# Kernel tuning notes

Hardware: AMD Instinct MI355X
Metric: run time of the kernel (lower is better)

Reference implementation:

```python
import jax, jax.numpy as jnp
import numpy as np

S = 7
NUM_CLASSES = 20
BATCH = 16384


def _iou(a, b):
    # a, b: [..., 4] boxes in (cx, cy, w, h) format
    ax1, ay1 = a[..., 0] - a[..., 2] / 2, a[..., 1] - a[..., 3] / 2
    ax2, ay2 = a[..., 0] + a[..., 2] / 2, a[..., 1] + a[..., 3] / 2
    bx1, by1 = b[..., 0] - b[..., 2] / 2, b[..., 1] - b[..., 3] / 2
    bx2, by2 = b[..., 0] + b[..., 2] / 2, b[..., 1] + b[..., 3] / 2
    iw = jnp.clip(jnp.minimum(ax2, bx2) - jnp.maximum(ax1, bx1), 0.0)
    ih = jnp.clip(jnp.minimum(ay2, by2) - jnp.maximum(ay1, by1), 0.0)
    inter = iw * ih
    union = a[..., 2] * a[..., 3] + b[..., 2] * b[..., 3] - inter
    return inter / (union + 1e-10)


def setup_inputs() -> dict:
    key = jax.random.key(0)
    k1, k2, k3, k4 = jax.random.split(key, 4)
    preds = jax.random.uniform(k1, (BATCH, S, S, 30), jnp.float32, 0.05, 0.95)
    box = jax.random.uniform(k2, (BATCH, S, S, 4), jnp.float32, 0.05, 0.95)
    conf = jax.random.bernoulli(k3, 0.3, (BATCH, S, S, 1)).astype(jnp.float32)
    cls = jax.random.uniform(k4, (BATCH, S, S, NUM_CLASSES), jnp.float32)
    labels = jnp.concatenate([box, conf, box, conf, cls], axis=-1)
    return {"preds": preds, "labels": labels}


def reference(preds, labels):
    obj = labels[..., 4] == 1.0          # [N, S, S] responsible-cell mask
    obj_f = obj.astype(preds.dtype)
    noobj_f = 1.0 - obj_f

    iou1 = _iou(preds[..., 0:4], labels[..., 0:4])
    iou2 = _iou(preds[..., 5:9], labels[..., 0:4])
    b1 = iou1 > iou2                      # box 1 is responsible
    b1f = b1.astype(preds.dtype)[..., None]

    # responsible / other box slices selected per cell
    p_xy = b1f * preds[..., 0:2] + (1 - b1f) * preds[..., 5:7]
    l_xy = b1f * labels[..., 0:2] + (1 - b1f) * labels[..., 5:7]
    p_wh = b1f * preds[..., 2:4] + (1 - b1f) * preds[..., 7:9]
    l_wh = b1f * labels[..., 2:4] + (1 - b1f) * labels[..., 7:9]
    conf_resp = jnp.where(b1, preds[..., 4], preds[..., 9])
    conf_other = jnp.where(b1, preds[..., 9], preds[..., 4])
    iou_resp = jnp.where(b1, iou1, iou2)
    iou_other = jnp.where(b1, iou2, iou1)

    loss_xy = 5.0 * jnp.sum(obj_f * jnp.sum((p_xy - l_xy) ** 2, axis=-1))
    loss_wh = jnp.sum(obj_f * jnp.sum((jnp.sqrt(p_wh) - jnp.sqrt(l_wh)) ** 2, axis=-1))
    loss_obj = jnp.sum(obj_f * (conf_resp - iou_resp) ** 2)
    loss_noobj_in = 0.5 * jnp.sum(obj_f * (conf_other - iou_other) ** 2)
    loss_noobj_out = 0.5 * jnp.sum(noobj_f * (preds[..., 4] ** 2 + preds[..., 9] ** 2))
    loss_cls = jnp.sum(obj_f * jnp.sum((preds[..., 10:] - labels[..., 10:]) ** 2, axis=-1))

    total = loss_xy + loss_wh + loss_obj + loss_noobj_in + loss_noobj_out + loss_cls
    return total / preds.shape[0]
```

## Files before the change

kernel.cpp:

```cpp
#include <hip/hip_runtime.h>

#define S 7
#define NUM_CLASSES 20
#define BATCH 16384
#define NCELLS (BATCH * S * S)
#define CPB 128
#define NTILES (NCELLS / CPB)
#define BLOCK 64
#define GRID 512
#define TILE_FLOATS (CPB * 30)
#define GPL 15

__device__ __forceinline__ void async_load16(const float* g, float* s) {
    __builtin_amdgcn_global_load_lds(
        (const __attribute__((address_space(1))) void*)g,
        (__attribute__((address_space(3))) void*)s,
        16, 0, 0);
}

__device__ __forceinline__ float iou_f(float acx, float acy, float aw, float ah,
                                       float bcx, float bcy, float bw, float bh) {
    float ax1 = acx - aw * 0.5f, ay1 = acy - ah * 0.5f;
    float ax2 = acx + aw * 0.5f, ay2 = acy + ah * 0.5f;
    float bx1 = bcx - bw * 0.5f, by1 = bcy - bh * 0.5f;
    float bx2 = bcx + bw * 0.5f, by2 = bcy + bh * 0.5f;
    float iw = fminf(ax2, bx2) - fmaxf(ax1, bx1);
    iw = fmaxf(iw, 0.0f);
    float ih = fminf(ay2, by2) - fmaxf(ay1, by1);
    ih = fmaxf(ih, 0.0f);
    float inter = iw * ih;
    float uni = aw * ah + bw * bh - inter;
    return inter / (uni + 1e-10f);
}

__device__ __forceinline__ float cell_loss(const float* cp, const float* cl) {
    float p[30], l[30];
    const float2* pp = (const float2*)cp;
    const float2* ll = (const float2*)cl;
#pragma unroll
    for (int j = 0; j < 15; ++j) {
        float2 v = pp[j];
        p[2 * j] = v.x; p[2 * j + 1] = v.y;
        float2 w = ll[j];
        l[2 * j] = w.x; l[2 * j + 1] = w.y;
    }

    float obj = (l[4] == 1.0f) ? 1.0f : 0.0f;

    float iou1 = iou_f(p[0], p[1], p[2], p[3], l[0], l[1], l[2], l[3]);
    float iou2 = iou_f(p[5], p[6], p[7], p[8], l[0], l[1], l[2], l[3]);
    bool b1 = iou1 > iou2;

    float pxy0 = b1 ? p[0] : p[5];
    float pxy1 = b1 ? p[1] : p[6];
    float pwh0 = b1 ? p[2] : p[7];
    float pwh1 = b1 ? p[3] : p[8];
    float conf_resp  = b1 ? p[4] : p[9];
    float conf_other = b1 ? p[9] : p[4];
    float iou_resp   = b1 ? iou1 : iou2;
    float iou_other  = b1 ? iou2 : iou1;

    float dx = pxy0 - l[0];
    float dy = pxy1 - l[1];
    float loss_xy = dx * dx + dy * dy;

    float sw0 = sqrtf(pwh0) - sqrtf(l[2]);
    float sw1 = sqrtf(pwh1) - sqrtf(l[3]);
    float loss_wh = sw0 * sw0 + sw1 * sw1;

    float d_obj = conf_resp - iou_resp;
    float loss_obj = d_obj * d_obj;

    float d_no = conf_other - iou_other;
    float loss_noobj_in = 0.5f * d_no * d_no;

    float loss_noobj_out = 0.5f * (1.0f - obj) * (p[4] * p[4] + p[9] * p[9]);

    float loss_cls = 0.0f;
#pragma unroll
    for (int c = 10; c < 30; ++c) {
        float d = p[c] - l[c];
        loss_cls += d * d;
    }

    return obj * (5.0f * loss_xy + loss_wh + loss_obj + loss_noobj_in + loss_cls)
         + loss_noobj_out;
}

__global__ __launch_bounds__(BLOCK) void yolo_loss_kernel(
        const float* __restrict__ preds,
        const float* __restrict__ labels,
        float* __restrict__ out) {
    __shared__ __align__(16) float sp[2][TILE_FLOATS];
    __shared__ __align__(16) float sl[2][TILE_FLOATS];

    const int lane = threadIdx.x;
    float acc = 0.0f;

    const int f0 = lane * 4;

    int t = blockIdx.x;
    const int iters = (NTILES - (int)blockIdx.x + GRID - 1) / GRID;

    {
        const float* gp = preds  + (size_t)t * TILE_FLOATS;
        const float* gl = labels + (size_t)t * TILE_FLOATS;
#pragma unroll
        for (int it = 0; it < GPL; ++it) {
            int f = f0 + it * 256;
            async_load16(gp + f, &sp[0][f]);
            async_load16(gl + f, &sl[0][f]);
        }
    }

    int bb = 0;
    for (int i = 1; i < iters; ++i) {
        const int tn = t + GRID;
        const float* gp = preds  + (size_t)tn * TILE_FLOATS;
        const float* gl = labels + (size_t)tn * TILE_FLOATS;
#pragma unroll
        for (int it = 0; it < GPL; ++it) {
            int f = f0 + it * 256;
            async_load16(gp + f, &sp[bb ^ 1][f]);
            async_load16(gl + f, &sl[bb ^ 1][f]);
        }
        asm volatile("s_waitcnt vmcnt(30)" ::: "memory");
        __builtin_amdgcn_sched_barrier(0);

        acc += cell_loss(&sp[bb][lane * 30],        &sl[bb][lane * 30]);
        acc += cell_loss(&sp[bb][(lane + 64) * 30], &sl[bb][(lane + 64) * 30]);

        t = tn;
        bb ^= 1;
    }

    asm volatile("s_waitcnt vmcnt(0)" ::: "memory");
    __builtin_amdgcn_sched_barrier(0);
    acc += cell_loss(&sp[bb][lane * 30],        &sl[bb][lane * 30]);
    acc += cell_loss(&sp[bb][(lane + 64) * 30], &sl[bb][(lane + 64) * 30]);

#pragma unroll
    for (int off = 32; off > 0; off >>= 1)
        acc += __shfl_down(acc, off, 64);
    if (lane == 0)
        atomicAdd(out, acc * (1.0f / (float)BATCH));
}

extern "C" void kernel_launch(void* const* d_in, const int* in_sizes, int n_in,
                              void* d_out, int out_size, void* d_ws, size_t ws_size,
                              hipStream_t stream) {
    const float* preds  = (const float*)d_in[0];
    const float* labels = (const float*)d_in[1];
    float* out = (float*)d_out;

    hipMemsetAsync(out, 0, sizeof(float), stream);

    yolo_loss_kernel<<<GRID, BLOCK, 0, stream>>>(preds, labels, out);
}
```

Before: 208.8 us.

## Replace async LDS double buffering with register-staged loads and more blocks

Drops the global_load_lds double-buffered pipeline and instead loads each 64-cell tile into registers as coalesced float4/float2 reads, writes it to a single LDS buffer, syncs, and computes one cell per thread. Tile size is halved and the grid is quadrupled, with a launch-bounds hint, so occupancy and memory-level parallelism come from more concurrent waves rather than explicit prefetch. The cost is two barriers per tile, no overlap of load and compute within a block, and four times as many atomics.

Result: no change. 208.9 us (+0.0%).

```diff
diff --git a/kernel.cpp b/kernel.cpp
--- a/kernel.cpp
+++ b/kernel.cpp
@@ -4,19 +4,11 @@
 #define NUM_CLASSES 20
 #define BATCH 16384
 #define NCELLS (BATCH * S * S)
-#define CPB 128
+#define CPB 64
 #define NTILES (NCELLS / CPB)
 #define BLOCK 64
-#define GRID 512
+#define GRID 2048
 #define TILE_FLOATS (CPB * 30)
-#define GPL 15
-
-__device__ __forceinline__ void async_load16(const float* g, float* s) {
-    __builtin_amdgcn_global_load_lds(
-        (const __attribute__((address_space(1))) void*)g,
-        (__attribute__((address_space(3))) void*)s,
-        16, 0, 0);
-}
 
 __device__ __forceinline__ float iou_f(float acx, float acy, float aw, float ah,
                                        float bcx, float bcy, float bw, float bh) {
@@ -87,57 +79,43 @@
          + loss_noobj_out;
 }
 
-__global__ __launch_bounds__(BLOCK) void yolo_loss_kernel(
+__global__ __launch_bounds__(BLOCK, 2) void yolo_loss_kernel(
         const float* __restrict__ preds,
         const float* __restrict__ labels,
         float* __restrict__ out) {
-    __shared__ __align__(16) float sp[2][TILE_FLOATS];
-    __shared__ __align__(16) float sl[2][TILE_FLOATS];
+    __shared__ __align__(16) float sp[TILE_FLOATS];
+    __shared__ __align__(16) float sl[TILE_FLOATS];
 
     const int lane = threadIdx.x;
     float acc = 0.0f;
 
-    const int f0 = lane * 4;
-
-    int t = blockIdx.x;
-    const int iters = (NTILES - (int)blockIdx.x + GRID - 1) / GRID;
-
-    {
+    for (int t = blockIdx.x; t < NTILES; t += GRID) {
         const float* gp = preds  + (size_t)t * TILE_FLOATS;
         const float* gl = labels + (size_t)t * TILE_FLOATS;
+
+        float4 vp[7], vl[7];
 #pragma unroll
-        for (int it = 0; it < GPL; ++it) {
-            int f = f0 + it * 256;
-            async_load16(gp + f, &sp[0][f]);
-            async_load16(gl + f, &sl[0][f]);
+        for (int j = 0; j < 7; ++j) {
+            vp[j] = ((const float4*)gp)[j * 64 + lane];
+            vl[j] = ((const float4*)gl)[j * 64 + lane];
         }
+        float2 tp = ((const float2*)(gp + 1792))[lane];
+        float2 tl = ((const float2*)(gl + 1792))[lane];
+
+#pragma unroll
+        for (int j = 0; j < 7; ++j) {
+            ((float4*)sp)[j * 64 + lane] = vp[j];
+            ((float4*)sl)[j * 64 + lane] = vl[j];
+        }
+        ((float2*)(sp + 1792))[lane] = tp;
+        ((float2*)(sl + 1792))[lane] = tl;
+
+        __syncthreads();
+
+        acc += cell_loss(&sp[lane * 30], &sl[lane * 30]);
+
+        __syncthreads();
     }
-
-    int bb = 0;
-    for (int i = 1; i < iters; ++i) {
-        const int tn = t + GRID;
-        const float* gp = preds  + (size_t)tn * TILE_FLOATS;
-        const float* gl = labels + (size_t)tn * TILE_FLOATS;
-#pragma unroll
-        for (int it = 0; it < GPL; ++it) {
-            int f = f0 + it * 256;
-            async_load16(gp + f, &sp[bb ^ 1][f]);
-            async_load16(gl + f, &sl[bb ^ 1][f]);
-        }
-        asm volatile("s_waitcnt vmcnt(30)" ::: "memory");
-        __builtin_amdgcn_sched_barrier(0);
-
-        acc += cell_loss(&sp[bb][lane * 30],        &sl[bb][lane * 30]);
-        acc += cell_loss(&sp[bb][(lane + 64) * 30], &sl[bb][(lane + 64) * 30]);
-
-        t = tn;
-        bb ^= 1;
-    }
-
-    asm volatile("s_waitcnt vmcnt(0)" ::: "memory");
-    __builtin_amdgcn_sched_barrier(0);
-    acc += cell_loss(&sp[bb][lane * 30],        &sl[bb][lane * 30]);
-    acc += cell_loss(&sp[bb][(lane + 64) * 30], &sl[bb][(lane + 64) * 30]);
 
 #pragma unroll
     for (int off = 32; off > 0; off >>= 1)
```
